# Performance work log

Measured on AMD Instinct MI355X. Metric: run time of the kernel, lower is better.

## Reference

```python
import jax, jax.numpy as jnp
import numpy as np

START = 1
PAD = 0
EPS = 1e-5

V, E, H, ENC_H = 32000, 512, 1024, 1024
B, S_ENC, T = 64, 64, 32  # T = max_len + 1


def _batchnorm(x, gamma, beta):
    # training-mode BatchNorm1d: biased batch statistics over batch dim
    mu = jnp.mean(x, axis=0)
    var = jnp.var(x, axis=0)
    return (x - mu) * jax.lax.rsqrt(var + EPS) * gamma + beta


def setup_inputs() -> dict:
    key = jax.random.key(0)
    ks = jax.random.split(key, 20)
    s = lambda i, shape, sc=0.02: (jax.random.normal(ks[i], shape, jnp.float32) * sc)
    emb = s(0, (V, E), 0.02).at[PAD].set(0.0)
    inp = {
        "encoder_outputs": jax.random.normal(ks[1], (B, S_ENC, ENC_H), jnp.float32),
        "decoder_label": jax.random.randint(ks[2], (B, T), 0, V, jnp.int32),
        "encoder_hidden_state": jax.random.normal(ks[3], (1, B, H), jnp.float32),
        "answer_lens": jax.random.randint(ks[4], (B,), 1, T, jnp.int32),
        "emb": emb,
        "w_ih": s(5, (3 * H, E)),
        "w_hh": s(6, (3 * H, H)),
        "b_ih": jnp.zeros((3 * H,), jnp.float32),
        "b_hh": jnp.zeros((3 * H,), jnp.float32),
        "bn1_g": jnp.ones((ENC_H + H,), jnp.float32),
        "bn1_b": jnp.zeros((ENC_H + H,), jnp.float32),
        "W1": s(7, (ENC_H + H, H)),
        "b1": jnp.zeros((H,), jnp.float32),
        "bn2_g": jnp.ones((H,), jnp.float32),
        "bn2_b": jnp.zeros((H,), jnp.float32),
        "W2": s(8, (H, V)),
        "b2": jnp.zeros((V,), jnp.float32),
    }
    return inp


def _forward(encoder_outputs, decoder_label, encoder_hidden_state,
             emb, w_ih, w_hh, b_ih, b_hh,
             bn1_g, bn1_b, W1, b1, bn2_g, bn2_b, W2, b2):
    # teacher forcing: step-0 input is START, then label tokens shifted by one
    start = jnp.full((B, 1), START, decoder_label.dtype)
    tokens = jnp.concatenate([start, decoder_label[:, : T - 1]], axis=1)  # [B,T]
    x_emb = emb[tokens]  # [B,T,E]
    # precompute input-side GRU gates for all steps: [T,B,3H]
    gates_x = jnp.einsum("bte,ge->tbg", x_emb, w_ih) + b_ih
    h0 = encoder_hidden_state[0]  # [B,H]

    def step(h, gx):
        gh = h @ w_hh.T + b_hh
        xr, xz, xn = jnp.split(gx, 3, axis=-1)
        hr, hz, hn = jnp.split(gh, 3, axis=-1)
        r = jax.nn.sigmoid(xr + hr)
        z = jax.nn.sigmoid(xz + hz)
        n = jnp.tanh(xn + r * hn)
        h_new = (1.0 - z) * n + z * h  # [B,H]
        # dot attention of new hidden over encoder outputs
        scores = jnp.einsum("bh,bsh->bs", h_new, encoder_outputs)
        w = jax.nn.softmax(scores, axis=-1)
        ctx = jnp.einsum("bs,bsh->bh", w, encoder_outputs)
        feat = jnp.concatenate([h_new, ctx], axis=-1)  # [B, ENC_H+H]
        y = _batchnorm(feat, bn1_g, bn1_b)
        y = jax.nn.elu(y @ W1 + b1)
        y = _batchnorm(y, bn2_g, bn2_b)
        probs = jax.nn.softmax(y @ W2 + b2, axis=-1)  # [B,V]
        return h_new, probs

    h_last, probs_t = jax.lax.scan(step, h0, gates_x)
    decoder_outputs = jnp.transpose(probs_t, (1, 0, 2))  # [B,T,V]
    return decoder_outputs, h_last[None]


def reference(encoder_outputs, decoder_label, encoder_hidden_state, answer_lens,
              emb, w_ih, w_hh, b_ih, b_hh,
              bn1_g, bn1_b, W1, b1, bn2_g, bn2_b, W2, b2):
    return _forward(encoder_outputs, decoder_label, encoder_hidden_state,
                    emb, w_ih, w_hh, b_ih, b_hh,
                    bn1_g, bn1_b, W1, b1, bn2_g, bn2_b, W2, b2)
```

## Files before the change

### kernel.cpp

```cpp
#include <hip/hip_runtime.h>

typedef __bf16 bf16;
typedef bf16 bf16x8 __attribute__((ext_vector_type(8)));
typedef float f32x4 __attribute__((ext_vector_type(4)));
typedef unsigned int u32;

#define Vv 32000
#define Ee 512
#define Hh 1024
#define Bb 64
#define Ssz 64
#define Tt 32
#define TBm 2048
#define FFc 2048
#define G3c 3072
#define NBLKG 128

__device__ __forceinline__ float sigm(float x) { return 1.f / (1.f + expf(-x)); }

__device__ __forceinline__ uint4 gload_sc(const void* p) {
  uint4 d;
  asm volatile("global_load_dwordx4 %0, %1, off sc0 sc1" : "=v"(d) : "v"(p));
  return d;
}
__device__ __forceinline__ uint4 gload16(const void* p) {
  uint4 d;
  asm volatile("global_load_dwordx4 %0, %1, off" : "=v"(d) : "v"(p));
  return d;
}
__device__ __forceinline__ u32 gload_p32(const void* p) {
  u32 d;
  asm volatile("global_load_dword %0, %1, off" : "=v"(d) : "v"(p));
  return d;
}
__device__ __forceinline__ void gstore_p32(void* p, u32 v) {
  asm volatile("global_store_dword %0, %1, off" :: "v"(p), "v"(v) : "memory");
}
__device__ __forceinline__ void gstore_sc16(void* p, u32 v) {
  asm volatile("global_store_short %0, %1, off sc0 sc1" :: "v"(p), "v"(v) : "memory");
}

__global__ void zero_k(u32* __restrict__ p, int n) {
  int i = blockIdx.x * blockDim.x + threadIdx.x;
  if (i < n) p[i] = 0u;
}

__global__ void cvt_simple_k(const float* __restrict__ s, bf16* __restrict__ d, int n) {
  int stride = gridDim.x * blockDim.x;
  for (int i = blockIdx.x * blockDim.x + threadIdx.x; i < n; i += stride)
    d[i] = (bf16)s[i];
}

__global__ void cvt_split_k(const float* __restrict__ s, bf16* __restrict__ hi,
                            bf16* __restrict__ lo, int n) {
  int stride = gridDim.x * blockDim.x;
  for (int i = blockIdx.x * blockDim.x + threadIdx.x; i < n; i += stride) {
    float v = s[i];
    bf16 h = (bf16)v;
    hi[i] = h;
    lo[i] = (bf16)(v - (float)h);
  }
}

__global__ void transpose_cvt_k(const float* __restrict__ src, bf16* __restrict__ dst,
                                int R, int C) {
  __shared__ float tile[32][33];
  int bx = blockIdx.x * 32;
  int by = blockIdx.y * 32;
  int tx = threadIdx.x & 31, ty = threadIdx.x >> 5;
#pragma unroll
  for (int i = 0; i < 4; ++i) {
    int r = ty + i * 8;
    tile[r][tx] = src[(size_t)(by + r) * C + bx + tx];
  }
  __syncthreads();
#pragma unroll
  for (int i = 0; i < 4; ++i) {
    int r = ty + i * 8;
    dst[(size_t)(bx + r) * R + by + tx] = (bf16)tile[tx][r];
  }
}

__global__ void embed_k(const float* __restrict__ emb, const int* __restrict__ label,
                        bf16* __restrict__ xe) {
  int m = blockIdx.x;
  int t = m >> 6, b = m & 63;
  int tok = (t == 0) ? 1 : label[b * Tt + t - 1];
  const float* src = emb + (size_t)tok * Ee;
  bf16* dst = xe + (size_t)m * Ee;
  for (int e = threadIdx.x; e < Ee; e += blockDim.x) dst[e] = (bf16)src[e];
}

template <int MODE>
__global__ void __launch_bounds__(256) gemm_nt_k(
    const bf16* __restrict__ A, const bf16* __restrict__ Bt,
    const float* __restrict__ bias, float* __restrict__ C,
    int M, int N, int K) {
  __shared__ bf16 As[128 * 32];
  __shared__ bf16 Bs[128 * 32];
  const int tid = threadIdx.x;
  const int wv = tid >> 6, ln = tid & 63;
  const int wr = wv >> 1, wc = wv & 1;
  const int l15 = ln & 15, l4 = ln >> 4;

  int NX = gridDim.x, NY = gridDim.y;
  int nwg = NX * NY;
  int lin = blockIdx.x + blockIdx.y * NX;
  int bx, by;
  if ((nwg & 7) == 0) {
    int per = nwg >> 3;
    int virt = (lin & 7) * per + (lin >> 3);
    by = virt % NY;
    bx = virt / NY;
  } else {
    bx = blockIdx.x;
    by = blockIdx.y;
  }
  const int m0 = by * 128, n0 = bx * 128;

  const f32x4 vzero = {0.f, 0.f, 0.f, 0.f};
  f32x4 acc[4][4];
#pragma unroll
  for (int i = 0; i < 4; ++i) {
#pragma unroll
    for (int j = 0; j < 4; ++j) acc[i][j] = vzero;
  }

  const int nk = K >> 5;
  for (int kt = 0; kt < nk; ++kt) {
    const int k0 = kt << 5;
    __syncthreads();
#pragma unroll
    for (int it = 0; it < 2; ++it) {
      int c = tid + it * 256;
      int row = c >> 2, kc = (c & 3) << 3;
      *(uint4*)&As[row * 32 + kc] = *(const uint4*)(A + (size_t)(m0 + row) * K + k0 + kc);
      *(uint4*)&Bs[row * 32 + kc] = *(const uint4*)(Bt + (size_t)(n0 + row) * K + k0 + kc);
    }
    __syncthreads();
    bf16x8 af[4], bfv[4];
#pragma unroll
    for (int mt = 0; mt < 4; ++mt)
      af[mt] = *(const bf16x8*)&As[(wr * 64 + mt * 16 + l15) * 32 + l4 * 8];
#pragma unroll
    for (int nt = 0; nt < 4; ++nt)
      bfv[nt] = *(const bf16x8*)&Bs[(wc * 64 + nt * 16 + l15) * 32 + l4 * 8];
#pragma unroll
    for (int mt = 0; mt < 4; ++mt) {
#pragma unroll
      for (int nt = 0; nt < 4; ++nt)
        acc[mt][nt] = __builtin_amdgcn_mfma_f32_16x16x32_bf16(af[mt], bfv[nt], acc[mt][nt], 0, 0, 0);
    }
  }

#pragma unroll
  for (int mt = 0; mt < 4; ++mt) {
#pragma unroll
    for (int nt = 0; nt < 4; ++nt) {
      int col = wc * 64 + nt * 16 + l15;
      int n = n0 + col;
      float bv = bias[n];
#pragma unroll
      for (int r = 0; r < 4; ++r) {
        int row = wr * 64 + mt * 16 + l4 * 4 + r;
        int m = m0 + row;
        float v = acc[mt][nt][r] + bv;
        if (MODE == 1) v = (v > 0.f) ? v : expm1f(v);
        if (MODE == 2) {
          size_t R = (size_t)(m & 63) * Tt + (size_t)(m >> 6);
          ((bf16*)C)[2 * R * (size_t)Vv + (size_t)n] = (bf16)v;
        } else {
          C[(size_t)m * N + n] = v;
        }
      }
    }
  }
}


#define ISSUE_CH(B, c)                                              \
  _Pragma("unroll")                                                 \
  for (int q = 0; q < 4; ++q) {                                     \
    int kk = (c) * 4 + q;                                           \
    int ke = kk * 32 + l4 * 8;                                      \
    B##h[q] = gload_sc(hhi + hrow + ke);                            \
    B##l[q] = gload_sc(hlo + hrow + ke);                            \
    B##w0[q] = gload16(w0p + kk * 32);                              \
    B##w1[q] = gload16(w1p + kk * 32);                              \
  }

#define COMP_CH(B, c)                                               \
  _Pragma("unroll")                                                 \
  for (int q = 0; q < 4; ++q) {                                     \
    int kk = (c) * 4 + q;                                           \
    int sb = (kk * 4 + l4) << 4;                                    \
    bf16x8 bhi0 = *(const bf16x8*)(ldsW + rowoff0 + (sb ^ xor0));   \
    bf16x8 bhi1 = *(const bf16x8*)(ldsW + 32768 + rowoff1 + (sb ^ xor0)); \
    bf16x8 ahi = __builtin_bit_cast(bf16x8, B##h[q]);               \
    bf16x8 alo = __builtin_bit_cast(bf16x8, B##l[q]);               \
    bf16x8 w0v = __builtin_bit_cast(bf16x8, B##w0[q]);              \
    bf16x8 w1v = __builtin_bit_cast(bf16x8, B##w1[q]);              \
    acc0 = __builtin_amdgcn_mfma_f32_16x16x32_bf16(ahi, bhi0, acc0, 0, 0, 0); \
    acx0 = __builtin_amdgcn_mfma_f32_16x16x32_bf16(ahi, w0v, acx0, 0, 0, 0);  \
    acx0 = __builtin_amdgcn_mfma_f32_16x16x32_bf16(alo, bhi0, acx0, 0, 0, 0); \
    acc1 = __builtin_amdgcn_mfma_f32_16x16x32_bf16(ahi, bhi1, acc1, 0, 0, 0); \
    acx1 = __builtin_amdgcn_mfma_f32_16x16x32_bf16(ahi, w1v, acx1, 0, 0, 0);  \
    acx1 = __builtin_amdgcn_mfma_f32_16x16x32_bf16(alo, bhi1, acx1, 0, 0, 0); \
  }

#define WAIT16 { asm volatile("s_waitcnt vmcnt(16)" ::: "memory"); __builtin_amdgcn_sched_barrier(0); }
#define WAIT0  { asm volatile("s_waitcnt vmcnt(0)" ::: "memory");  __builtin_amdgcn_sched_barrier(0); }

__global__ void __launch_bounds__(256, 1) gru_all_k(
    const bf16* __restrict__ hHi0, const bf16* __restrict__ hLo0,
    bf16* __restrict__ hHi1, bf16* __restrict__ hLo1,
    const bf16* __restrict__ whhHi, const bf16* __restrict__ whhLo,
    const float* __restrict__ gates, const float* __restrict__ bhh,
    const float* __restrict__ h0, float* __restrict__ hseq,
    u32* __restrict__ bar) {
  __shared__ __align__(16) char ldsW[49152];
  const int tid = threadIdx.x;
  const int wv = tid >> 6, ln = tid & 63;
  const int l15 = ln & 15, l4 = ln >> 4;
  const int bid = blockIdx.x;
  const int j8 = bid * 8;

  for (int idx = tid; idx < 24 * 128; idx += 256) {
    int row = idx >> 7;
    int seg = idx & 127;
    int grow = (row < 8) ? (j8 + row)
             : (row < 16) ? (Hh + j8 + row - 8)
                          : (2 * Hh + j8 + row - 16);
    int rr = (row < 16) ? row : (row - 16);
    int region = (row < 16) ? 0 : 32768;
    int dst = region + rr * 2048 + ((seg * 16) ^ ((rr & 7) << 4));
    *(uint4*)(ldsW + dst) = *(const uint4*)(whhHi + (size_t)grow * Hh + seg * 8);
  }
  __syncthreads();

  const int rowoff0 = l15 * 2048;
  const int rowoff1 = (l15 & 7) * 2048;
  const int xor0 = (l15 & 7) << 4;

  const int cA = l15;
  const int grow0 = (cA < 8) ? (j8 + cA) : (Hh + j8 + cA - 8);
  const int grow1 = 2 * Hh + j8 + (cA & 7);
  const bf16* w0p = whhLo + (size_t)grow0 * Hh + l4 * 8;
  const bf16* w1p = whhLo + (size_t)grow1 * Hh + l4 * 8;

  const size_t hrow = (size_t)(wv * 16 + l15) * Hh;

  const int jj = j8 + (cA & 7);
  int gbr[4];
#pragma unroll
  for (int r = 0; r < 4; ++r) gbr[r] = wv * 16 + (ln >> 4) * 4 + r;
  const float* gAddr[4];
#pragma unroll
  for (int r = 0; r < 4; ++r) gAddr[r] = gates + (size_t)gbr[r] * G3c + jj;
  const float bhr = bhh[jj], bhz = bhh[Hh + jj], bhn = bhh[2 * Hh + jj];
  float hp[4];
#pragma unroll
  for (int r = 0; r < 4; ++r) hp[r] = h0[(size_t)gbr[r] * Hh + jj];

  const bf16* HIc[2] = {hHi0, hHi1};
  const bf16* LOc[2] = {hLo0, hLo1};
  bf16* HIm[2] = {(bf16*)hHi0, hHi1};
  bf16* LOm[2] = {(bf16*)hLo0, hLo1};
  const f32x4 vzero = {0.f, 0.f, 0.f, 0.f};

  for (int t = 0; t < Tt; ++t) {
    const bf16* hhi = HIc[t & 1];
    const bf16* hlo = LOc[t & 1];
    f32x4 acc0 = vzero, acx0 = vzero, acc1 = vzero, acx1 = vzero;
    uint4 Ah[4], Al[4], Aw0[4], Aw1[4];
    uint4 Bh[4], Bl[4], Bw0[4], Bw1[4];
    uint4 Ch[4], Cl[4], Cw0[4], Cw1[4];

    u32 gR[4], gZ[4], gN[4];
    const size_t gt = (size_t)t * Bb * G3c;
#pragma unroll
    for (int r = 0; r < 4; ++r) {
      gR[r] = gload_p32(gAddr[r] + gt);
      gZ[r] = gload_p32(gAddr[r] + gt + Hh);
      gN[r] = gload_p32(gAddr[r] + gt + 2 * Hh);
    }

    ISSUE_CH(A, 0) ISSUE_CH(B, 1) WAIT16
    COMP_CH(A, 0)  ISSUE_CH(C, 2) WAIT16
    COMP_CH(B, 1)  ISSUE_CH(A, 3) WAIT16
    COMP_CH(C, 2)  ISSUE_CH(B, 4) WAIT16
    COMP_CH(A, 3)  ISSUE_CH(C, 5) WAIT16
    COMP_CH(B, 4)  ISSUE_CH(A, 6) WAIT16
    COMP_CH(C, 5)  ISSUE_CH(B, 7) WAIT16
    COMP_CH(A, 6)  WAIT0
    COMP_CH(B, 7)

    float s0r[4], s1r[4], sZ[4];
#pragma unroll
    for (int r = 0; r < 4; ++r) {
      s0r[r] = acc0[r] + acx0[r];
      s1r[r] = acc1[r] + acx1[r];
    }
#pragma unroll
    for (int r = 0; r < 4; ++r) sZ[r] = __shfl_xor(s0r[r], 8);

    if (cA < 8) {
      float* hout = hseq + (size_t)t * Bb * Hh;
      bf16* nhi = HIm[(t + 1) & 1];
      bf16* nlo = LOm[(t + 1) & 1];
#pragma unroll
      for (int r = 0; r < 4; ++r) {
        float rg = sigm(__builtin_bit_cast(float, gR[r]) + s0r[r] + bhr);
        float zg = sigm(__builtin_bit_cast(float, gZ[r]) + sZ[r] + bhz);
        float ng = tanhf(__builtin_bit_cast(float, gN[r]) + rg * (s1r[r] + bhn));
        float hv = (1.f - zg) * ng + zg * hp[r];
        hp[r] = hv;
        size_t o = (size_t)gbr[r] * Hh + jj;
        gstore_p32(hout + o, __builtin_bit_cast(u32, hv));
        bf16 hb = (bf16)hv;
        bf16 lb = (bf16)(hv - (float)hb);
        gstore_sc16(nhi + o, (u32)__builtin_bit_cast(unsigned short, hb));
        gstore_sc16(nlo + o, (u32)__builtin_bit_cast(unsigned short, lb));
      }
    }

    if (t < Tt - 1) {
      __syncthreads();
      if (tid == 0) {
        __hip_atomic_fetch_add(bar + (bid & 7) * 32, 1u,
                               __ATOMIC_RELAXED, __HIP_MEMORY_SCOPE_AGENT);
      }
      if (wv == 0) {
        unsigned target = (unsigned)(t + 1) * (NBLKG / 8);
        bool ok;
        do {
          unsigned v = 0xFFFFFFFFu;
          if (ln < 8)
            v = __hip_atomic_load(bar + ln * 32, __ATOMIC_RELAXED,
                                  __HIP_MEMORY_SCOPE_AGENT);
          ok = __all((ln >= 8) || (v >= target));
          if (!ok) __builtin_amdgcn_s_sleep(1);
        } while (!ok);
      }
      __syncthreads();
    }
  }
}

__global__ void __launch_bounds__(256) attn_k(
    const float* __restrict__ hseq, const float* __restrict__ enc,
    float* __restrict__ feat) {
  __shared__ float red[256];
  __shared__ float wsm[Ssz];
  int m = blockIdx.x;
  int t = m >> 6, b = m & 63;
  const float* hv = hseq + (size_t)t * Bb * Hh + (size_t)b * Hh;
  const float* eb = enc + (size_t)b * Ssz * Hh;
  int tid = threadIdx.x;
  int s = tid >> 2, q = tid & 3;
  const float* er = eb + (size_t)s * Hh + q * 256;
  const float* hq = hv + q * 256;
  float p = 0.f;
#pragma unroll 4
  for (int i = 0; i < 256; i += 4) {
    float4 a = *(const float4*)(hq + i);
    float4 c = *(const float4*)(er + i);
    p += a.x * c.x + a.y * c.y + a.z * c.z + a.w * c.w;
  }
  red[tid] = p;
  __syncthreads();
  if (tid < 64) {
    float sc = red[tid * 4] + red[tid * 4 + 1] + red[tid * 4 + 2] + red[tid * 4 + 3];
    float mx = sc;
#pragma unroll
    for (int off = 32; off > 0; off >>= 1) mx = fmaxf(mx, __shfl_xor(mx, off));
    float e = expf(sc - mx);
    float sm = e;
#pragma unroll
    for (int off = 32; off > 0; off >>= 1) sm += __shfl_xor(sm, off);
    wsm[tid] = e / sm;
  }
  __syncthreads();
  float* fr = feat + (size_t)m * FFc;
  for (int h = tid; h < Hh; h += 256) {
    float a = 0.f;
#pragma unroll 8
    for (int si = 0; si < Ssz; ++si) a = fmaf(wsm[si], eb[(size_t)si * Hh + h], a);
    fr[Hh + h] = a;
    fr[h] = hv[h];
  }
}

__global__ void __launch_bounds__(256) bn_k(
    const float* __restrict__ x, const float* __restrict__ gam,
    const float* __restrict__ bet, bf16* __restrict__ y, int CH) {
  int t = blockIdx.y;
  int c = blockIdx.x * 256 + threadIdx.x;
  const float* xp = x + (size_t)t * Bb * CH + c;
  float v[Bb];
  float s = 0.f, ss = 0.f;
#pragma unroll
  for (int b = 0; b < Bb; ++b) {
    float u = xp[(size_t)b * CH];
    v[b] = u;
    s += u;
    ss += u * u;
  }
  float mean = s * (1.f / Bb);
  float var = ss * (1.f / Bb) - mean * mean;
  float inv = rsqrtf(var + 1e-5f);
  float sc = gam[c] * inv;
  float sh = bet[c] - mean * sc;
  bf16* yp = y + (size_t)t * Bb * CH + c;
#pragma unroll
  for (int b = 0; b < Bb; ++b) yp[(size_t)b * CH] = (bf16)(v[b] * sc + sh);
}

__global__ void __launch_bounds__(256) softmax_k(float* __restrict__ out) {
  __shared__ float rm[256], rs[256];
  int m = blockIdx.x;
  int t = m >> 6, b = m & 63;
  size_t R = (size_t)b * Tt + t;
  const bf16* rin = (const bf16*)out + 2 * R * (size_t)Vv;
  float* rout = out + R * (size_t)Vv;
  int tid = threadIdx.x;
  uint4 v[16];
  float mx = -3.0e38f, sm = 0.f;
#pragma unroll
  for (int j = 0; j < 16; ++j) {
    int i = tid * 8 + j * 2048;
    if (i < Vv) {
      v[j] = *(const uint4*)(rin + i);
      const bf16* pv = (const bf16*)&v[j];
      float f0 = (float)pv[0], f1 = (float)pv[1], f2 = (float)pv[2], f3 = (float)pv[3];
      float f4 = (float)pv[4], f5 = (float)pv[5], f6 = (float)pv[6], f7 = (float)pv[7];
      float m8 = fmaxf(fmaxf(fmaxf(f0, f1), fmaxf(f2, f3)),
                       fmaxf(fmaxf(f4, f5), fmaxf(f6, f7)));
      if (m8 > mx) { sm *= expf(mx - m8); mx = m8; }
      sm += expf(f0 - mx) + expf(f1 - mx) + expf(f2 - mx) + expf(f3 - mx)
          + expf(f4 - mx) + expf(f5 - mx) + expf(f6 - mx) + expf(f7 - mx);
    }
  }
  rm[tid] = mx;
  rs[tid] = sm;
  __syncthreads();
  for (int off = 128; off > 0; off >>= 1) {
    if (tid < off) {
      float ma = rm[tid], mb = rm[tid + off];
      float m2 = fmaxf(ma, mb);
      rs[tid] = rs[tid] * expf(ma - m2) + rs[tid + off] * expf(mb - m2);
      rm[tid] = m2;
    }
    __syncthreads();
  }
  float M = rm[0];
  float inv = 1.f / rs[0];
#pragma unroll
  for (int j = 0; j < 16; ++j) {
    int i = tid * 8 + j * 2048;
    if (i < Vv) {
      const bf16* pv = (const bf16*)&v[j];
      float4 o0, o1;
      o0.x = expf((float)pv[0] - M) * inv;
      o0.y = expf((float)pv[1] - M) * inv;
      o0.z = expf((float)pv[2] - M) * inv;
      o0.w = expf((float)pv[3] - M) * inv;
      o1.x = expf((float)pv[4] - M) * inv;
      o1.y = expf((float)pv[5] - M) * inv;
      o1.z = expf((float)pv[6] - M) * inv;
      o1.w = expf((float)pv[7] - M) * inv;
      *(float4*)(rout + i) = o0;
      *(float4*)(rout + i + 4) = o1;
    }
  }
}

__global__ void hlast_k(const float* __restrict__ src, float* __restrict__ dst) {
  int i = blockIdx.x * 256 + threadIdx.x;
  dst[i] = src[i];
}

extern "C" void kernel_launch(void* const* d_in, const int* in_sizes, int n_in,
                              void* d_out, int out_size, void* d_ws, size_t ws_size,
                              hipStream_t stream) {
  const float* enc   = (const float*)d_in[0];
  const int*   label = (const int*)d_in[1];
  const float* h0    = (const float*)d_in[2];
  const float* emb   = (const float*)d_in[4];
  const float* w_ih  = (const float*)d_in[5];
  const float* w_hh  = (const float*)d_in[6];
  const float* b_ih  = (const float*)d_in[7];
  const float* b_hh  = (const float*)d_in[8];
  const float* bn1g  = (const float*)d_in[9];
  const float* bn1b  = (const float*)d_in[10];
  const float* W1    = (const float*)d_in[11];
  const float* b1    = (const float*)d_in[12];
  const float* bn2g  = (const float*)d_in[13];
  const float* bn2b  = (const float*)d_in[14];
  const float* W2    = (const float*)d_in[15];
  const float* b2    = (const float*)d_in[16];
  float* out = (float*)d_out;
  (void)in_sizes; (void)n_in; (void)out_size; (void)ws_size;

  char* ws = (char*)d_ws;
  size_t off = 0;
  auto alloc = [&](size_t bytes) -> void* {
    void* p = ws + off;
    off += (bytes + 255) & ~(size_t)255;
    return p;
  };
  bf16*  W2t   = (bf16*)alloc((size_t)Vv * Hh * 2);
  bf16*  W1t   = (bf16*)alloc((size_t)Hh * FFc * 2);
  bf16*  wihB  = (bf16*)alloc((size_t)G3c * Ee * 2);
  bf16*  whhHi = (bf16*)alloc((size_t)G3c * Hh * 2);
  bf16*  whhLo = (bf16*)alloc((size_t)G3c * Hh * 2);
  bf16*  xeB   = (bf16*)alloc((size_t)TBm * Ee * 2);
  float* gates = (float*)alloc((size_t)TBm * G3c * 4);
  float* hseq  = (float*)alloc((size_t)Tt * Bb * Hh * 4);
  bf16*  hHi0  = (bf16*)alloc((size_t)Bb * Hh * 2);
  bf16*  hHi1  = (bf16*)alloc((size_t)Bb * Hh * 2);
  bf16*  hLo0  = (bf16*)alloc((size_t)Bb * Hh * 2);
  bf16*  hLo1  = (bf16*)alloc((size_t)Bb * Hh * 2);
  u32*   bar   = (u32*)alloc(2048);
  float* feat  = gates;
  bf16*  featB = (bf16*)alloc((size_t)TBm * FFc * 2);
  float* Y     = (float*)alloc((size_t)TBm * Hh * 4);
  bf16*  ybB   = (bf16*)alloc((size_t)TBm * Hh * 2);

  zero_k<<<1, 512, 0, stream>>>(bar, 512);

  cvt_simple_k<<<1024, 256, 0, stream>>>(w_ih, wihB, G3c * Ee);
  cvt_split_k<<<2048, 256, 0, stream>>>(w_hh, whhHi, whhLo, G3c * Hh);
  transpose_cvt_k<<<dim3(Hh / 32, FFc / 32), 256, 0, stream>>>(W1, W1t, FFc, Hh);
  transpose_cvt_k<<<dim3(Vv / 32, Hh / 32), 256, 0, stream>>>(W2, W2t, Hh, Vv);
  embed_k<<<TBm, 128, 0, stream>>>(emb, label, xeB);
  cvt_split_k<<<256, 256, 0, stream>>>(h0, hHi0, hLo0, Bb * Hh);

  gemm_nt_k<0><<<dim3(G3c / 128, TBm / 128), 256, 0, stream>>>(
      xeB, wihB, b_ih, gates, TBm, G3c, Ee);

  gru_all_k<<<NBLKG, 256, 0, stream>>>(
      hHi0, hLo0, hHi1, hLo1, whhHi, whhLo, gates, b_hh, h0, hseq, bar);

  attn_k<<<TBm, 256, 0, stream>>>(hseq, enc, feat);
  bn_k<<<dim3(FFc / 256, Tt), 256, 0, stream>>>(feat, bn1g, bn1b, featB, FFc);
  gemm_nt_k<1><<<dim3(Hh / 128, TBm / 128), 256, 0, stream>>>(
      featB, W1t, b1, Y, TBm, Hh, FFc);
  bn_k<<<dim3(Hh / 256, Tt), 256, 0, stream>>>(Y, bn2g, bn2b, ybB, Hh);
  gemm_nt_k<2><<<dim3(Vv / 128, TBm / 128), 256, 0, stream>>>(
      ybB, W2t, b2, out, TBm, Vv, Hh);
  softmax_k<<<TBm, 256, 0, stream>>>(out);
  hlast_k<<<(Bb * Hh) / 256, 256, 0, stream>>>(
      hseq + (size_t)(Tt - 1) * Bb * Hh, out + (size_t)Bb * Tt * Vv);
}
```

Before: 1.163 ms.

## Split GRU recurrent matvec K dimension across two wave groups per block

The persistent GRU kernel now launches 512 threads per block, and the 8 waves split the hidden-size reduction into two K halves of 512. Each wave runs half as many load/MFMA chunks. The upper half writes its partial sums to an LDS scratch area, and after a block barrier the lower half adds them and applies the gate update. This shortens the serial per-step critical path of the recurrence by doubling the waves working on it, at the cost of an extra __syncthreads and LDS traffic each step, plus higher register pressure from the 512-thread launch bound.

```diff
diff --git a/kernel.cpp b/kernel.cpp
--- a/kernel.cpp
+++ b/kernel.cpp
@@ -182,7 +182,7 @@
   _Pragma("unroll")                                                 \
   for (int q = 0; q < 4; ++q) {                                     \
     int kk = (c) * 4 + q;                                           \
-    int ke = kk * 32 + l4 * 8;                                      \
+    int ke = kbase + kk * 32 + l4 * 8;                              \
     B##h[q] = gload_sc(hhi + hrow + ke);                            \
     B##l[q] = gload_sc(hlo + hrow + ke);                            \
     B##w0[q] = gload16(w0p + kk * 32);                              \
@@ -193,9 +193,9 @@
   _Pragma("unroll")                                                 \
   for (int q = 0; q < 4; ++q) {                                     \
     int kk = (c) * 4 + q;                                           \
-    int sb = (kk * 4 + l4) << 4;                                    \
-    bf16x8 bhi0 = *(const bf16x8*)(ldsW + rowoff0 + (sb ^ xor0));   \
-    bf16x8 bhi1 = *(const bf16x8*)(ldsW + 32768 + rowoff1 + (sb ^ xor0)); \
+    int sb = kb2 + (((kk * 4 + l4) << 4) ^ xor0);                   \
+    bf16x8 bhi0 = *(const bf16x8*)(ldsW + rowoff0 + sb);            \
+    bf16x8 bhi1 = *(const bf16x8*)(ldsW + 32768 + rowoff1 + sb);    \
     bf16x8 ahi = __builtin_bit_cast(bf16x8, B##h[q]);               \
     bf16x8 alo = __builtin_bit_cast(bf16x8, B##l[q]);               \
     bf16x8 w0v = __builtin_bit_cast(bf16x8, B##w0[q]);              \
@@ -211,21 +211,26 @@
 #define WAIT16 { asm volatile("s_waitcnt vmcnt(16)" ::: "memory"); __builtin_amdgcn_sched_barrier(0); }
 #define WAIT0  { asm volatile("s_waitcnt vmcnt(0)" ::: "memory");  __builtin_amdgcn_sched_barrier(0); }
 
-__global__ void __launch_bounds__(256, 1) gru_all_k(
+__global__ void __launch_bounds__(512, 1) gru_all_k(
     const bf16* __restrict__ hHi0, const bf16* __restrict__ hLo0,
     bf16* __restrict__ hHi1, bf16* __restrict__ hLo1,
     const bf16* __restrict__ whhHi, const bf16* __restrict__ whhLo,
     const float* __restrict__ gates, const float* __restrict__ bhh,
     const float* __restrict__ h0, float* __restrict__ hseq,
     u32* __restrict__ bar) {
-  __shared__ __align__(16) char ldsW[49152];
+  __shared__ __align__(16) char ldsW[49152 + 8192];
+  float* sred = (float*)(ldsW + 49152);
   const int tid = threadIdx.x;
   const int wv = tid >> 6, ln = tid & 63;
   const int l15 = ln & 15, l4 = ln >> 4;
   const int bid = blockIdx.x;
   const int j8 = bid * 8;
-
-  for (int idx = tid; idx < 24 * 128; idx += 256) {
+  const int btile = wv & 3;
+  const int khalf = wv >> 2;
+  const int kbase = khalf * 512;
+  const int kb2 = kbase * 2;
+
+  for (int idx = tid; idx < 24 * 128; idx += 512) {
     int row = idx >> 7;
     int seg = idx & 127;
     int grow = (row < 8) ? (j8 + row)
@@ -245,15 +250,15 @@
   const int cA = l15;
   const int grow0 = (cA < 8) ? (j8 + cA) : (Hh + j8 + cA - 8);
   const int grow1 = 2 * Hh + j8 + (cA & 7);
-  const bf16* w0p = whhLo + (size_t)grow0 * Hh + l4 * 8;
-  const bf16* w1p = whhLo + (size_t)grow1 * Hh + l4 * 8;
-
-  const size_t hrow = (size_t)(wv * 16 + l15) * Hh;
+  const bf16* w0p = whhLo + (size_t)grow0 * Hh + kbase + l4 * 8;
+  const bf16* w1p = whhLo + (size_t)grow1 * Hh + kbase + l4 * 8;
+
+  const size_t hrow = (size_t)(btile * 16 + l15) * Hh;
 
   const int jj = j8 + (cA & 7);
   int gbr[4];
 #pragma unroll
-  for (int r = 0; r < 4; ++r) gbr[r] = wv * 16 + (ln >> 4) * 4 + r;
+  for (int r = 0; r < 4; ++r) gbr[r] = btile * 16 + l4 * 4 + r;
   const float* gAddr[4];
 #pragma unroll
   for (int r = 0; r < 4; ++r) gAddr[r] = gates + (size_t)gbr[r] * G3c + jj;
@@ -288,39 +293,43 @@
     ISSUE_CH(A, 0) ISSUE_CH(B, 1) WAIT16
     COMP_CH(A, 0)  ISSUE_CH(C, 2) WAIT16
     COMP_CH(B, 1)  ISSUE_CH(A, 3) WAIT16
-    COMP_CH(C, 2)  ISSUE_CH(B, 4) WAIT16
-    COMP_CH(A, 3)  ISSUE_CH(C, 5) WAIT16
-    COMP_CH(B, 4)  ISSUE_CH(A, 6) WAIT16
-    COMP_CH(C, 5)  ISSUE_CH(B, 7) WAIT16
-    COMP_CH(A, 6)  WAIT0
-    COMP_CH(B, 7)
-
-    float s0r[4], s1r[4], sZ[4];
-#pragma unroll
-    for (int r = 0; r < 4; ++r) {
-      s0r[r] = acc0[r] + acx0[r];
-      s1r[r] = acc1[r] + acx1[r];
-    }
-#pragma unroll
-    for (int r = 0; r < 4; ++r) sZ[r] = __shfl_xor(s0r[r], 8);
-
-    if (cA < 8) {
-      float* hout = hseq + (size_t)t * Bb * Hh;
-      bf16* nhi = HIm[(t + 1) & 1];
-      bf16* nlo = LOm[(t + 1) & 1];
-#pragma unroll
-      for (int r = 0; r < 4; ++r) {
-        float rg = sigm(__builtin_bit_cast(float, gR[r]) + s0r[r] + bhr);
-        float zg = sigm(__builtin_bit_cast(float, gZ[r]) + sZ[r] + bhz);
-        float ng = tanhf(__builtin_bit_cast(float, gN[r]) + rg * (s1r[r] + bhn));
-        float hv = (1.f - zg) * ng + zg * hp[r];
-        hp[r] = hv;
-        size_t o = (size_t)gbr[r] * Hh + jj;
-        gstore_p32(hout + o, __builtin_bit_cast(u32, hv));
-        bf16 hb = (bf16)hv;
-        bf16 lb = (bf16)(hv - (float)hb);
-        gstore_sc16(nhi + o, (u32)__builtin_bit_cast(unsigned short, hb));
-        gstore_sc16(nlo + o, (u32)__builtin_bit_cast(unsigned short, lb));
+    COMP_CH(C, 2)  WAIT0
+    COMP_CH(A, 3)
+
+    f32x4 s0 = acc0 + acx0;
+    f32x4 s1 = acc1 + acx1;
+    if (khalf == 1) {
+      *(f32x4*)&sred[(btile * 2 + 0) * 256 + ln * 4] = s0;
+      *(f32x4*)&sred[(btile * 2 + 1) * 256 + ln * 4] = s1;
+    }
+    __syncthreads();
+    if (khalf == 0) {
+      s0 += *(const f32x4*)&sred[(btile * 2 + 0) * 256 + ln * 4];
+      s1 += *(const f32x4*)&sred[(btile * 2 + 1) * 256 + ln * 4];
+      float s0r[4], s1r[4], sZ[4];
+#pragma unroll
+      for (int r = 0; r < 4; ++r) { s0r[r] = s0[r]; s1r[r] = s1[r]; }
+#pragma unroll
+      for (int r = 0; r < 4; ++r) sZ[r] = __shfl_xor(s0r[r], 8);
+
+      if (cA < 8) {
+        float* hout = hseq + (size_t)t * Bb * Hh;
+        bf16* nhi = HIm[(t + 1) & 1];
+        bf16* nlo = LOm[(t + 1) & 1];
+#pragma unroll
+        for (int r = 0; r < 4; ++r) {
+          float rg = sigm(__builtin_bit_cast(float, gR[r]) + s0r[r] + bhr);
+          float zg = sigm(__builtin_bit_cast(float, gZ[r]) + sZ[r] + bhz);
+          float ng = tanhf(__builtin_bit_cast(float, gN[r]) + rg * (s1r[r] + bhn));
+          float hv = (1.f - zg) * ng + zg * hp[r];
+          hp[r] = hv;
+          size_t o = (size_t)gbr[r] * Hh + jj;
+          gstore_p32(hout + o, __builtin_bit_cast(u32, hv));
+          bf16 hb = (bf16)hv;
+          bf16 lb = (bf16)(hv - (float)hb);
+          gstore_sc16(nhi + o, (u32)__builtin_bit_cast(unsigned short, hb));
+          gstore_sc16(nlo + o, (u32)__builtin_bit_cast(unsigned short, lb));
+        }
       }
     }
 
@@ -539,7 +548,7 @@
   gemm_nt_k<0><<<dim3(G3c / 128, TBm / 128), 256, 0, stream>>>(
       xeB, wihB, b_ih, gates, TBm, G3c, Ee);
 
-  gru_all_k<<<NBLKG, 256, 0, stream>>>(
+  gru_all_k<<<NBLKG, 512, 0, stream>>>(
       hHi0, hLo0, hHi1, hLo1, whhHi, whhLo, gates, b_hh, h0, hseq, bar);
 
   attn_k<<<TBm, 256, 0, stream>>>(hseq, enc, feat);
```

Result: slower. 1.287 ms (+10.6%).
